# Performance work log

Hardware: AMD Instinct MI355X
Metric: run time of the kernel (lower is better)

Reference implementation:

```python
import jax, jax.numpy as jnp
import numpy as np

N, E, B = 20000, 320000, 64
H, D = 4, 64          # heads, out_channels per head
HD = H * D            # 256
F_IN = 4
NUM_ACTIONS = 100
NEG_SLOPE = 0.2


def _lin(k, fan_in, fan_out, scale=0.05):
    kw, kb = jax.random.split(k)
    return (jax.random.normal(kw, (fan_in, fan_out), jnp.float32) * scale,
            jax.random.normal(kb, (fan_out,), jnp.float32) * scale)


def setup_inputs() -> dict:
    key = jax.random.key(0)
    ks = jax.random.split(key, 32)
    x = jax.random.normal(ks[0], (N, F_IN), jnp.float32)
    edge_index = jax.random.randint(ks[1], (2, E), 0, N)
    edge_attr = jax.random.normal(ks[2], (E, 1), jnp.float32)
    batch_idx = jnp.sort(jax.random.randint(ks[3], (N,), 0, B))
    action = jax.random.randint(ks[4], (B,), 0, NUM_ACTIONS)

    # GATv2 layer 1 (in=4)
    Wl1, bl1 = _lin(ks[5], F_IN, HD)
    Wr1, br1 = _lin(ks[6], F_IN, HD)
    We1 = jax.random.normal(ks[7], (1, HD), jnp.float32) * 0.05
    att1 = jax.random.normal(ks[8], (H, D), jnp.float32) * 0.05
    b1 = jnp.zeros((HD,), jnp.float32)
    # GATv2 layer 2 (in=256)
    Wl2, bl2 = _lin(ks[9], HD, HD)
    Wr2, br2 = _lin(ks[10], HD, HD)
    We2 = jax.random.normal(ks[11], (1, HD), jnp.float32) * 0.05
    att2 = jax.random.normal(ks[12], (H, D), jnp.float32) * 0.05
    b2 = jnp.zeros((HD,), jnp.float32)
    # critic MLP 256->128->64->1
    Wc1, bc1 = _lin(ks[13], 256, 128)
    Wc2, bc2 = _lin(ks[14], 128, 64)
    Wc3, bc3 = _lin(ks[15], 64, 1)
    # actor MLP 256->128->64->num_actions
    Wa1, ba1 = _lin(ks[16], 256, 128)
    Wa2, ba2 = _lin(ks[17], 128, 64)
    Wa3, ba3 = _lin(ks[18], 64, NUM_ACTIONS)
    return dict(x=x, edge_index=edge_index, edge_attr=edge_attr, batch_idx=batch_idx,
                action=action,
                Wl1=Wl1, bl1=bl1, Wr1=Wr1, br1=br1, We1=We1, att1=att1, b1=b1,
                Wl2=Wl2, bl2=bl2, Wr2=Wr2, br2=br2, We2=We2, att2=att2, b2=b2,
                Wc1=Wc1, bc1=bc1, Wc2=Wc2, bc2=bc2, Wc3=Wc3, bc3=bc3,
                Wa1=Wa1, ba1=ba1, Wa2=Wa2, ba2=ba2, Wa3=Wa3, ba3=ba3)


def gatv2(x, src, dst, edge_attr, Wl, bl, Wr, br, We, att, bias):
    n = x.shape[0]
    xl = (x @ Wl + bl).reshape(n, H, D)   # source transform (messages)
    xr = (x @ Wr + br).reshape(n, H, D)   # target transform
    e = (edge_attr @ We).reshape(-1, H, D)
    m = xl[src] + xr[dst] + e             # [E,H,D]
    s = jnp.sum(jax.nn.leaky_relu(m, NEG_SLOPE) * att, axis=-1)  # [E,H]
    smax = jax.ops.segment_max(s, dst, num_segments=n)
    a = jnp.exp(s - smax[dst])
    denom = jax.ops.segment_sum(a, dst, num_segments=n)
    alpha = a / (denom[dst] + 1e-16)      # scatter-softmax over in-edges
    out = jax.ops.segment_sum(alpha[..., None] * xl[src], dst, num_segments=n)
    return out.reshape(n, HD) + bias


def mlp3(f, W1, b1, W2, b2, W3, b3):
    h = jax.nn.relu(f @ W1 + b1)
    h = jax.nn.relu(h @ W2 + b2)
    return h @ W3 + b3


def reference(x, edge_index, edge_attr, batch_idx, action,
              Wl1, bl1, Wr1, br1, We1, att1, b1,
              Wl2, bl2, Wr2, br2, We2, att2, b2,
              Wc1, bc1, Wc2, bc2, Wc3, bc3,
              Wa1, ba1, Wa2, ba2, Wa3, ba3):
    src, dst = edge_index[0], edge_index[1]
    h = jax.nn.relu(gatv2(x, src, dst, edge_attr, Wl1, bl1, Wr1, br1, We1, att1, b1))
    h = jax.nn.relu(gatv2(h, src, dst, edge_attr, Wl2, bl2, Wr2, br2, We2, att2, b2))
    # global mean pool over graphs
    sums = jax.ops.segment_sum(h, batch_idx, num_segments=B)
    cnts = jax.ops.segment_sum(jnp.ones((h.shape[0],), h.dtype), batch_idx, num_segments=B)
    feats = sums / jnp.maximum(cnts, 1.0)[:, None]          # [B,256]
    logits = mlp3(feats, Wa1, ba1, Wa2, ba2, Wa3, ba3)       # [B,A]
    value = mlp3(feats, Wc1, bc1, Wc2, bc2, Wc3, bc3)        # [B,1]
    logp = jax.nn.log_softmax(logits, axis=-1)
    log_prob = jnp.take_along_axis(logp, action[:, None], axis=-1)[:, 0]
    entropy = -jnp.sum(jnp.exp(logp) * logp, axis=-1)
    return logits, log_prob, entropy, value
```

## Files before the change

### kernel.cpp

```cpp
#include <hip/hip_runtime.h>
#include <hip/hip_bf16.h>
#include <cstddef>

typedef __hip_bfloat16 bf16;
typedef unsigned short u16;
typedef __attribute__((ext_vector_type(8))) short short8;
typedef __attribute__((ext_vector_type(4))) float float4v;
typedef __attribute__((ext_vector_type(2))) float float2v;

#define HD 256
#define A_MAX 128

static __device__ __forceinline__ float b2f(const bf16 v) { return __bfloat162float(v); }
static __device__ __forceinline__ bf16 f2b(float v) { return __float2bfloat16(v); }

static __device__ __forceinline__ float2v up2(unsigned int u) {
  union { unsigned int i; float f; } a, b;
  a.i = u << 16; b.i = u & 0xffff0000u;
  float2v r; r.x = a.f; r.y = b.f; return r;
}

static __device__ __forceinline__ float ldf(const void* p, size_t i, bool f32) {
  return f32 ? ((const float*)p)[i] : b2f(((const bf16*)p)[i]);
}
template <bool F32>
static __device__ __forceinline__ float ldt(const void* p, size_t i) {
  return F32 ? ((const float*)p)[i] : b2f(((const bf16*)p)[i]);
}
static __device__ __forceinline__ void stf(void* p, size_t i, bool f32, float v) {
  if (f32) ((float*)p)[i] = v;
  else     ((bf16*)p)[i] = f2b(v);
}

__global__ void k_sentinel(float* out, int n, float v) {
  int i = blockIdx.x * blockDim.x + threadIdx.x;
  if (i < n) out[i] = v;
}

__global__ void k_init(const u16* __restrict__ xbits, int* __restrict__ flag,
                       int* deg, int N) {
  int i = blockIdx.x * blockDim.x + threadIdx.x;
  if (blockIdx.x == 0 && threadIdx.x < 64) {
    int l = threadIdx.x;
    int huge = 0;
    for (int k = l; k < 256; k += 64) {
      u16 u = xbits[2 * k];
      int ex = (u >> 7) & 0xFF;
      if (ex >= 0xB0) huge++;
    }
#pragma unroll
    for (int off = 32; off > 0; off >>= 1) huge += __shfl_xor(huge, off, 64);
    if (l == 0) *flag = (huge >= 20) ? 1 : 0;
  }
  if (i < N) deg[i] = 0;
}

__global__ void k_hist(const int* __restrict__ dst, int* __restrict__ deg, int E) {
  int e = blockIdx.x * blockDim.x + threadIdx.x;
  if (e < E) atomicAdd(&deg[dst[e]], 1);
}

__global__ void k_scan(const int* __restrict__ deg, int* __restrict__ offs, int n) {
  __shared__ int wsum[17];
  __shared__ int carry_s;
  int t = threadIdx.x, w = t >> 6, l = t & 63;
  if (t == 0) carry_s = 0;
  __syncthreads();
  for (int base = 0; base < n; base += 1024) {
    int i = base + t;
    int v = (i < n) ? deg[i] : 0;
    int x = v;
#pragma unroll
    for (int off = 1; off < 64; off <<= 1) {
      int y = __shfl_up(x, off, 64);
      if (l >= off) x += y;
    }
    if (l == 63) wsum[w] = x;
    __syncthreads();
    if (t == 0) {
      int s = 0;
#pragma unroll
      for (int k = 0; k < 16; k++) { int tmp = wsum[k]; wsum[k] = s; s += tmp; }
      wsum[16] = s;
    }
    __syncthreads();
    int c = carry_s;
    if (i < n) offs[i] = c + wsum[w] + x - v;
    __syncthreads();
    if (t == 0) carry_s = c + wsum[16];
    __syncthreads();
  }
  if (t == 0) offs[n] = carry_s;
}

__global__ void k_misc(const int* __restrict__ src, const int* __restrict__ dst,
                       const void* __restrict__ ea, int* __restrict__ offs,
                       int2* __restrict__ csr,
                       const void* __restrict__ x,
                       const void* __restrict__ Wl1, const void* __restrict__ bl1,
                       const void* __restrict__ Wr1, const void* __restrict__ br1,
                       bf16* __restrict__ P, bf16* __restrict__ Q,
                       const void* __restrict__ Wl2, const void* __restrict__ Wr2,
                       const void* __restrict__ bl2, const void* __restrict__ br2,
                       bf16* __restrict__ Wfrag, bf16* __restrict__ bias2,
                       const int* __restrict__ flag,
                       int E, int N, int nSc, int nX1) {
  bool f32 = flag[0] != 0;
  int b = blockIdx.x, t = threadIdx.x;
  if (b < nSc) {
    int e = b * 256 + t;
    if (e >= E) return;
    int d = dst[e];
    int pos = atomicAdd(&offs[d], 1);
    int2 v;
    v.x = src[e];
    v.y = __float_as_int(ldf(ea, e, f32));
    csr[pos] = v;
  } else if (b < nSc + nX1) {
    int n0 = (b - nSc) * 4;
    float wl0 = ldf(Wl1, t, f32),          wl1 = ldf(Wl1, HD + t, f32);
    float wl2 = ldf(Wl1, 2 * HD + t, f32), wl3 = ldf(Wl1, 3 * HD + t, f32);
    float wr0 = ldf(Wr1, t, f32),          wr1 = ldf(Wr1, HD + t, f32);
    float wr2 = ldf(Wr1, 2 * HD + t, f32), wr3 = ldf(Wr1, 3 * HD + t, f32);
    float bbl = ldf(bl1, t, f32), bbr = ldf(br1, t, f32);
#pragma unroll
    for (int k = 0; k < 4; k++) {
      int n = n0 + k;
      if (n >= N) break;
      float x0 = ldf(x, (size_t)n * 4 + 0, f32), x1 = ldf(x, (size_t)n * 4 + 1, f32);
      float x2 = ldf(x, (size_t)n * 4 + 2, f32), x3 = ldf(x, (size_t)n * 4 + 3, f32);
      P[(size_t)n * HD + t] = f2b(bbl + x0 * wl0 + x1 * wl1 + x2 * wl2 + x3 * wl3);
      Q[(size_t)n * HD + t] = f2b(bbr + x0 * wr0 + x1 * wr1 + x2 * wr2 + x3 * wr3);
    }
  } else {
    int pb = b - nSc - nX1;
    int ct = pb >> 3, kt = pb & 7;
    if (pb == 0) {
      bias2[t]       = f2b(ldf(bl2, t, f32));
      bias2[t + 256] = f2b(ldf(br2, t, f32));
    }
#pragma unroll
    for (int half = 0; half < 2; half++) {
      int e = half * 256 + t;
      int m = e & 15;
      int rest = e >> 4;
      int quad = rest >> 3, j = rest & 7;
      int l = quad * 16 + m;
      int k = kt * 32 + quad * 8 + j;
      int n = ct * 16 + m;
      const void* W = (n < 256) ? Wl2 : Wr2;
      float v = ldf(W, (size_t)k * 256 + (n & 255), f32);
      Wfrag[(size_t)pb * 512 + l * 8 + j] = f2b(v);
    }
  }
}

__global__ __launch_bounds__(256) void k_xform2_mfma(
    const bf16* __restrict__ hin, const bf16* __restrict__ Wfrag,
    const bf16* __restrict__ bias2,
    bf16* __restrict__ P, bf16* __restrict__ Q, int N) {
  int w = threadIdx.x >> 6, l = threadIdx.x & 63;
  int r0 = blockIdx.x * 16;
  if (r0 >= N) return;
  int m = l & 15;
  int quad = l >> 4;
  int row = r0 + m;
  if (row >= N) row = N - 1;

  short8 a[8];
  const u16* arow = (const u16*)hin + (size_t)row * 256;
#pragma unroll
  for (int kt = 0; kt < 8; kt++)
    a[kt] = *(const short8*)(arow + kt * 32 + quad * 8);

#pragma unroll
  for (int ct = 0; ct < 8; ct++) {
    int c_tile = w * 8 + ct;
    int c = c_tile * 16 + m;
    const u16* bbase = (const u16*)Wfrag + ((size_t)c_tile * 8) * 512 + l * 8;
    float4v acc = {0.f, 0.f, 0.f, 0.f};
#pragma unroll
    for (int kt = 0; kt < 8; kt++) {
      short8 b = *(const short8*)(bbase + kt * 512);
      acc = __builtin_amdgcn_mfma_f32_16x16x32_bf16(a[kt], b, acc, 0, 0, 0);
    }
    float bv = b2f(bias2[c]);
#pragma unroll
    for (int i = 0; i < 4; i++) {
      int r = r0 + quad * 4 + i;
      if (r < N) {
        float v = acc[i] + bv;
        if (c < 256) P[(size_t)r * 256 + c] = f2b(v);
        else         Q[(size_t)r * 256 + (c - 256)] = f2b(v);
      }
    }
  }
}

__global__ __launch_bounds__(256) void k_gat(
    const bf16* __restrict__ xl, const bf16* __restrict__ xr,
    const int2* __restrict__ csr, const int* __restrict__ offs,
    const void* __restrict__ We, const void* __restrict__ att,
    const void* __restrict__ bias,
    bf16* __restrict__ hout, const int* __restrict__ flag, int N) {
  int w = threadIdx.x >> 6, l = threadIdx.x & 63;
  int n = blockIdx.x * 4 + w;
  if (n >= N) return;
  bool f32 = flag[0] != 0;
  int d0 = l << 2;

  uint2 xu = *(const uint2*)((const u16*)xr + (size_t)n * HD + d0);
  float2v xr01 = up2(xu.x), xr23 = up2(xu.y);
  float2v We01, We23, at01, at23;
  We01.x = ldf(We, d0 + 0, f32); We01.y = ldf(We, d0 + 1, f32);
  We23.x = ldf(We, d0 + 2, f32); We23.y = ldf(We, d0 + 3, f32);
  at01.x = ldf(att, d0 + 0, f32); at01.y = ldf(att, d0 + 1, f32);
  at23.x = ldf(att, d0 + 2, f32); at23.y = ldf(att, d0 + 3, f32);

  int beg = (n > 0) ? offs[n - 1] : 0;
  int end = offs[n];
  float2v acc01 = {0.f, 0.f}, acc23 = {0.f, 0.f};
  float dn = 0.f;

  int j = beg;
  for (; j + 4 <= end; j += 4) {
    int2 v[4];
#pragma unroll
    for (int q = 0; q < 4; q++) v[q] = csr[j + q];
    uint2 su[4];
#pragma unroll
    for (int q = 0; q < 4; q++)
      su[q] = *(const uint2*)((const u16*)xl + (size_t)v[q].x * HD + d0);
    float2v x01[4], x23[4];
    float ps[4];
#pragma unroll
    for (int q = 0; q < 4; q++) {
      x01[q] = up2(su[q].x); x23[q] = up2(su[q].y);
      float eav = __int_as_float(v[q].y);
      float2v ev; ev.x = eav; ev.y = eav;
      float2v m01 = x01[q] + xr01 + ev * We01;
      float2v m23 = x23[q] + xr23 + ev * We23;
      float2v lr01, lr23;
      lr01.x = fmaxf(m01.x, 0.2f * m01.x); lr01.y = fmaxf(m01.y, 0.2f * m01.y);
      lr23.x = fmaxf(m23.x, 0.2f * m23.x); lr23.y = fmaxf(m23.y, 0.2f * m23.y);
      float2v pp = lr01 * at01 + lr23 * at23;
      ps[q] = pp.x + pp.y;
    }
#pragma unroll
    for (int off = 1; off <= 8; off <<= 1) {
#pragma unroll
      for (int q = 0; q < 4; q++) ps[q] += __shfl_xor(ps[q], off, 64);
    }
#pragma unroll
    for (int q = 0; q < 4; q++) {
      float a = __expf(fminf(fmaxf(ps[q], -40.f), 40.f));
      dn += a;
      float2v av; av.x = a; av.y = a;
      acc01 += av * x01[q];
      acc23 += av * x23[q];
    }
  }
  for (; j < end; j++) {
    int2 v = csr[j];
    float eav = __int_as_float(v.y);
    uint2 su = *(const uint2*)((const u16*)xl + (size_t)v.x * HD + d0);
    float2v x01 = up2(su.x), x23 = up2(su.y);
    float2v ev; ev.x = eav; ev.y = eav;
    float2v m01 = x01 + xr01 + ev * We01;
    float2v m23 = x23 + xr23 + ev * We23;
    float2v lr01, lr23;
    lr01.x = fmaxf(m01.x, 0.2f * m01.x); lr01.y = fmaxf(m01.y, 0.2f * m01.y);
    lr23.x = fmaxf(m23.x, 0.2f * m23.x); lr23.y = fmaxf(m23.y, 0.2f * m23.y);
    float2v pp = lr01 * at01 + lr23 * at23;
    float ps = pp.x + pp.y;
    ps += __shfl_xor(ps, 1, 64);
    ps += __shfl_xor(ps, 2, 64);
    ps += __shfl_xor(ps, 4, 64);
    ps += __shfl_xor(ps, 8, 64);
    float a = __expf(fminf(fmaxf(ps, -40.f), 40.f));
    dn += a;
    float2v av; av.x = a; av.y = a;
    acc01 += av * x01;
    acc23 += av * x23;
  }

  float inv = 1.f / (dn + 1e-16f);
  bf16 o[4];
  o[0] = f2b(fmaxf(acc01.x * inv + ldf(bias, d0 + 0, f32), 0.f));
  o[1] = f2b(fmaxf(acc01.y * inv + ldf(bias, d0 + 1, f32), 0.f));
  o[2] = f2b(fmaxf(acc23.x * inv + ldf(bias, d0 + 2, f32), 0.f));
  o[3] = f2b(fmaxf(acc23.y * inv + ldf(bias, d0 + 3, f32), 0.f));
  *(ushort4*)((u16*)hout + (size_t)n * HD + d0) = *(ushort4*)o;
}


static __device__ __forceinline__ int lb(const int* a, int n, int v) {
  int lo = 0, hi = n;
  while (lo < hi) { int m = (lo + hi) >> 1; if (a[m] < v) lo = m + 1; else hi = m; }
  return lo;
}

template <bool F32>
static __device__ void mlp_body(const bf16* __restrict__ R,
                                const int* __restrict__ bidx, int N,
                                const int* __restrict__ act,
                                const void* Wa1, const void* ba1, const void* Wa2, const void* ba2,
                                const void* Wa3, const void* ba3,
                                const void* Wc1, const void* bc1, const void* Wc2, const void* bc2,
                                const void* Wc3, const void* bc3,
                                void* __restrict__ out, int B, int A) {
  __shared__ float f[HD];
  __shared__ float p1[2][128];
  __shared__ float h1[128];
  __shared__ float p2[4][64];
  __shared__ float h2[64];
  __shared__ float lg[A_MAX];
  __shared__ float sc[2];
  int blk = blockIdx.x, g = blk >> 1, which = blk & 1, t = threadIdx.x;
  int s_ = lb(bidx, N, g), e_ = lb(bidx, N, g + 1);
  float inv = 1.f / fmaxf((float)(e_ - s_), 1.f);
  {
    float a0 = 0.f, a1 = 0.f, a2 = 0.f, a3 = 0.f;
    int i = s_;
    for (; i + 4 <= e_; i += 4) {
      a0 += b2f(R[(size_t)(i + 0) * HD + t]);
      a1 += b2f(R[(size_t)(i + 1) * HD + t]);
      a2 += b2f(R[(size_t)(i + 2) * HD + t]);
      a3 += b2f(R[(size_t)(i + 3) * HD + t]);
    }
    for (; i < e_; i++) a0 += b2f(R[(size_t)i * HD + t]);
    f[t] = ((a0 + a1) + (a2 + a3)) * inv;
  }
  __syncthreads();

  const void *W1 = which ? Wc1 : Wa1, *B1 = which ? bc1 : ba1;
  const void *W2 = which ? Wc2 : Wa2, *B2 = which ? bc2 : ba2;

  {
    int j = t & 127, half = t >> 7;
    int i0 = half * 128;
    float a0 = 0.f, a1 = 0.f, a2 = 0.f, a3 = 0.f;
    for (int u = 0; u < 128; u += 4) {
      a0 += f[i0 + u + 0] * ldt<F32>(W1, (size_t)(i0 + u + 0) * 128 + j);
      a1 += f[i0 + u + 1] * ldt<F32>(W1, (size_t)(i0 + u + 1) * 128 + j);
      a2 += f[i0 + u + 2] * ldt<F32>(W1, (size_t)(i0 + u + 2) * 128 + j);
      a3 += f[i0 + u + 3] * ldt<F32>(W1, (size_t)(i0 + u + 3) * 128 + j);
    }
    p1[half][j] = (a0 + a1) + (a2 + a3);
  }
  __syncthreads();
  if (t < 128) h1[t] = fmaxf(p1[0][t] + p1[1][t] + ldt<F32>(B1, t), 0.f);
  __syncthreads();

  {
    int j = t & 63, q = t >> 6;
    int i0 = q * 32;
    float a0 = 0.f, a1 = 0.f;
    for (int u = 0; u < 32; u += 2) {
      a0 += h1[i0 + u + 0] * ldt<F32>(W2, (size_t)(i0 + u + 0) * 64 + j);
      a1 += h1[i0 + u + 1] * ldt<F32>(W2, (size_t)(i0 + u + 1) * 64 + j);
    }
    p2[q][j] = a0 + a1;
  }
  __syncthreads();
  if (t < 64) h2[t] = fmaxf(p2[0][t] + p2[1][t] + p2[2][t] + p2[3][t] + ldt<F32>(B2, t), 0.f);
  __syncthreads();

  if (which == 0) {
    if (t < A) {
      float a0 = 0.f, a1 = 0.f, a2 = 0.f, a3 = 0.f;
      for (int i = 0; i < 64; i += 4) {
        a0 += h2[i + 0] * ldt<F32>(Wa3, (size_t)(i + 0) * A + t);
        a1 += h2[i + 1] * ldt<F32>(Wa3, (size_t)(i + 1) * A + t);
        a2 += h2[i + 2] * ldt<F32>(Wa3, (size_t)(i + 2) * A + t);
        a3 += h2[i + 3] * ldt<F32>(Wa3, (size_t)(i + 3) * A + t);
      }
      lg[t] = (a0 + a1) + (a2 + a3) + ldt<F32>(ba3, t);
    }
    __syncthreads();
    if (t == 0) {
      float mx = -3.4e38f;
      for (int i = 0; i < A; i++) mx = fmaxf(mx, lg[i]);
      float s = 0.f;
      for (int i = 0; i < A; i++) s += __expf(lg[i] - mx);
      sc[0] = mx;
      sc[1] = logf(s);
    }
    __syncthreads();
    float mx = sc[0], lse = sc[1];
    if (t < A) stf(out, (size_t)g * A + t, F32, lg[t]);
    if (t == 0) {
      int a = act[g];
      stf(out, (size_t)B * A + g, F32, lg[a] - mx - lse);
      float ent = 0.f;
      for (int i = 0; i < A; i++) {
        float l = lg[i] - mx - lse;
        ent -= __expf(l) * l;
      }
      stf(out, (size_t)B * A + B + g, F32, ent);
    }
  } else {
    if (t < 64) {
      float v = h2[t] * ldt<F32>(Wc3, t);
#pragma unroll
      for (int off = 32; off > 0; off >>= 1) v += __shfl_xor(v, off, 64);
      if (t == 0) stf(out, (size_t)B * A + 2 * B + g, F32, v + ldt<F32>(bc3, 0));
    }
  }
}

__global__ void k_mlp(const bf16* __restrict__ R,
                      const int* __restrict__ bidx, int N,
                      const int* __restrict__ act,
                      const void* Wa1, const void* ba1, const void* Wa2, const void* ba2,
                      const void* Wa3, const void* ba3,
                      const void* Wc1, const void* bc1, const void* Wc2, const void* bc2,
                      const void* Wc3, const void* bc3,
                      void* __restrict__ out, const int* __restrict__ flag, int B, int A) {
  if (flag[0] != 0)
    mlp_body<true >(R, bidx, N, act, Wa1, ba1, Wa2, ba2, Wa3, ba3,
                    Wc1, bc1, Wc2, bc2, Wc3, bc3, out, B, A);
  else
    mlp_body<false>(R, bidx, N, act, Wa1, ba1, Wa2, ba2, Wa3, ba3,
                    Wc1, bc1, Wc2, bc2, Wc3, bc3, out, B, A);
}


extern "C" void kernel_launch(void* const* d_in, const int* in_sizes, int n_in,
                              void* d_out, int out_size, void* d_ws, size_t ws_size,
                              hipStream_t stream) {
  const void* x    = d_in[0];
  const int*  ei   = (const int*)d_in[1];
  const void* ea   = d_in[2];
  const int*  bidx = (const int*)d_in[3];
  const int*  act  = (const int*)d_in[4];
  const void *Wl1 = d_in[5],  *bl1 = d_in[6];
  const void *Wr1 = d_in[7],  *br1 = d_in[8];
  const void *We1 = d_in[9],  *att1 = d_in[10];
  const void *b1  = d_in[11];
  const void *Wl2 = d_in[12], *bl2 = d_in[13];
  const void *Wr2 = d_in[14], *br2 = d_in[15];
  const void *We2 = d_in[16], *att2 = d_in[17];
  const void *b2  = d_in[18];
  const void *Wc1 = d_in[19], *bc1 = d_in[20];
  const void *Wc2 = d_in[21], *bc2 = d_in[22];
  const void *Wc3 = d_in[23], *bc3 = d_in[24];
  const void *Wa1 = d_in[25], *ba1 = d_in[26];
  const void *Wa2 = d_in[27], *ba2 = d_in[28];
  const void *Wa3 = d_in[29], *ba3 = d_in[30];

  const int N = in_sizes[0] / 4;
  const int E = in_sizes[1] / 2;
  const int B = in_sizes[4];
  const int A = in_sizes[30];

  char* p = (char*)d_ws;
  auto carve = [&](size_t bytes) {
    void* r = (void*)p;
    p += (bytes + 255) & ~(size_t)255;
    return r;
  };
  int*   dflag   = (int*)carve(4);
  int*   deg     = (int*)carve((size_t)N * 4);
  int*   offs    = (int*)carve((size_t)(N + 1) * 4);
  int2*  csr     = (int2*)carve((size_t)E * 8);
  bf16*  P       = (bf16*)carve((size_t)N * HD * 2);
  bf16*  Q       = (bf16*)carve((size_t)N * HD * 2);
  bf16*  R       = (bf16*)carve((size_t)N * HD * 2);
  bf16*  Wfrag   = (bf16*)carve((size_t)512 * 256 * 2);
  bf16*  bias2   = (bf16*)carve((size_t)512 * 2);
  size_t need = (size_t)(p - (char*)d_ws);

  if (ws_size < need) {
    float v = 1000.f + (float)(ws_size >> 20);
    int n = out_size / 2;
    k_sentinel<<<(n + 255) / 256, 256, 0, stream>>>((float*)d_out, n, v);
    return;
  }

  const int* srcA = ei;
  const int* dstA = ei + E;

  int nSc = (E + 255) / 256;
  int nX1 = (N + 3) / 4;

  k_init<<<(N + 255) / 256, 256, 0, stream>>>((const u16*)x, dflag, deg, N);
  k_hist<<<(E + 255) / 256, 256, 0, stream>>>(dstA, deg, E);
  k_scan<<<1, 1024, 0, stream>>>(deg, offs, N);
  k_misc<<<nSc + nX1 + 256, 256, 0, stream>>>(srcA, dstA, ea, offs, csr,
                                              x, Wl1, bl1, Wr1, br1, P, Q,
                                              Wl2, Wr2, bl2, br2, Wfrag, bias2,
                                              dflag, E, N, nSc, nX1);
  k_gat<<<(N + 3) / 4, 256, 0, stream>>>(P, Q, csr, offs, We1, att1, b1, R, dflag, N);
  k_xform2_mfma<<<(N + 15) / 16, 256, 0, stream>>>(R, Wfrag, bias2, P, Q, N);
  k_gat<<<(N + 3) / 4, 256, 0, stream>>>(P, Q, csr, offs, We2, att2, b2, R, dflag, N);
  k_mlp<<<B * 2, 256, 0, stream>>>(R, bidx, N, act,
                                   Wa1, ba1, Wa2, ba2, Wa3, ba3,
                                   Wc1, bc1, Wc2, bc2, Wc3, bc3,
                                   d_out, dflag, B, A);
}
```

Before: 318.8 us.

## Parallelize degree scan across blocks and split mean-pool into separate kernel

Replaces the single-block serial prefix scan over node degrees with a three-kernel block-sum, block-offset and apply scan spread over many blocks. Moves global mean pooling out of the MLP kernel into a new pooling kernel where 16 blocks per graph each sum a strided subset of nodes into fp32 partials, which the MLP kernel then reduces. Both changes target serial phases that ran on few blocks. In exchange they add three extra kernel launches and a small partial-sum buffer in the workspace.

```diff
diff --git a/kernel.cpp b/kernel.cpp
--- a/kernel.cpp
+++ b/kernel.cpp
@@ -60,37 +60,53 @@
   if (e < E) atomicAdd(&deg[dst[e]], 1);
 }
 
-__global__ void k_scan(const int* __restrict__ deg, int* __restrict__ offs, int n) {
-  __shared__ int wsum[17];
-  __shared__ int carry_s;
-  int t = threadIdx.x, w = t >> 6, l = t & 63;
-  if (t == 0) carry_s = 0;
-  __syncthreads();
-  for (int base = 0; base < n; base += 1024) {
-    int i = base + t;
-    int v = (i < n) ? deg[i] : 0;
-    int x = v;
-#pragma unroll
-    for (int off = 1; off < 64; off <<= 1) {
-      int y = __shfl_up(x, off, 64);
-      if (l >= off) x += y;
-    }
-    if (l == 63) wsum[w] = x;
-    __syncthreads();
-    if (t == 0) {
-      int s = 0;
-#pragma unroll
-      for (int k = 0; k < 16; k++) { int tmp = wsum[k]; wsum[k] = s; s += tmp; }
-      wsum[16] = s;
-    }
-    __syncthreads();
-    int c = carry_s;
-    if (i < n) offs[i] = c + wsum[w] + x - v;
-    __syncthreads();
-    if (t == 0) carry_s = c + wsum[16];
-    __syncthreads();
-  }
-  if (t == 0) offs[n] = carry_s;
+__global__ void k_sumb(const int* __restrict__ deg, int* __restrict__ bsum, int n) {
+  __shared__ int ws[16];
+  int b = blockIdx.x, t = threadIdx.x;
+  int i = b * 1024 + t;
+  int v = (i < n) ? deg[i] : 0;
+#pragma unroll
+  for (int off = 32; off > 0; off >>= 1) v += __shfl_xor(v, off, 64);
+  if ((t & 63) == 0) ws[t >> 6] = v;
+  __syncthreads();
+  if (t == 0) {
+    int s = 0;
+#pragma unroll
+    for (int k = 0; k < 16; k++) s += ws[k];
+    bsum[b] = s;
+  }
+}
+
+__global__ void k_scanb(const int* __restrict__ bsum, int* __restrict__ boff,
+                        int nb, int* __restrict__ offs, int n) {
+  if (threadIdx.x == 0) {
+    int s = 0;
+    for (int i = 0; i < nb; i++) { boff[i] = s; s += bsum[i]; }
+    offs[n] = s;
+  }
+}
+
+__global__ void k_scanapply(const int* __restrict__ deg, const int* __restrict__ boff,
+                            int* __restrict__ offs, int n) {
+  __shared__ int wsum[16];
+  int b = blockIdx.x, t = threadIdx.x, w = t >> 6, l = t & 63;
+  int i = b * 1024 + t;
+  int v = (i < n) ? deg[i] : 0;
+  int x = v;
+#pragma unroll
+  for (int off = 1; off < 64; off <<= 1) {
+    int y = __shfl_up(x, off, 64);
+    if (l >= off) x += y;
+  }
+  if (l == 63) wsum[w] = x;
+  __syncthreads();
+  if (t == 0) {
+    int s = 0;
+#pragma unroll
+    for (int k = 0; k < 16; k++) { int tmp = wsum[k]; wsum[k] = s; s += tmp; }
+  }
+  __syncthreads();
+  if (i < n) offs[i] = boff[b] + wsum[w] + x - v;
 }
 
 __global__ void k_misc(const int* __restrict__ src, const int* __restrict__ dst,
@@ -300,8 +316,25 @@
   return lo;
 }
 
+__global__ void k_pool(const bf16* __restrict__ h, const int* __restrict__ bidx,
+                       float* __restrict__ feats16, int Bc, int N) {
+  int g = blockIdx.x >> 4, part = blockIdx.x & 15, t = threadIdx.x;
+  int s = lb(bidx, N, g), e_ = lb(bidx, N, g + 1);
+  float a0 = 0.f, a1 = 0.f, a2 = 0.f, a3 = 0.f;
+  int i = s + part;
+  for (; i + 48 < e_; i += 64) {
+    a0 += b2f(h[(size_t)(i +  0) * HD + t]);
+    a1 += b2f(h[(size_t)(i + 16) * HD + t]);
+    a2 += b2f(h[(size_t)(i + 32) * HD + t]);
+    a3 += b2f(h[(size_t)(i + 48) * HD + t]);
+  }
+  for (; i < e_; i += 16) a0 += b2f(h[(size_t)i * HD + t]);
+  feats16[((size_t)part * Bc + g) * HD + t] = (a0 + a1) + (a2 + a3);
+}
+
+
 template <bool F32>
-static __device__ void mlp_body(const bf16* __restrict__ R,
+static __device__ void mlp_body(const float* __restrict__ feats16,
                                 const int* __restrict__ bidx, int N,
                                 const int* __restrict__ act,
                                 const void* Wa1, const void* ba1, const void* Wa2, const void* ba2,
@@ -320,16 +353,15 @@
   int s_ = lb(bidx, N, g), e_ = lb(bidx, N, g + 1);
   float inv = 1.f / fmaxf((float)(e_ - s_), 1.f);
   {
-    float a0 = 0.f, a1 = 0.f, a2 = 0.f, a3 = 0.f;
-    int i = s_;
-    for (; i + 4 <= e_; i += 4) {
-      a0 += b2f(R[(size_t)(i + 0) * HD + t]);
-      a1 += b2f(R[(size_t)(i + 1) * HD + t]);
-      a2 += b2f(R[(size_t)(i + 2) * HD + t]);
-      a3 += b2f(R[(size_t)(i + 3) * HD + t]);
-    }
-    for (; i < e_; i++) a0 += b2f(R[(size_t)i * HD + t]);
-    f[t] = ((a0 + a1) + (a2 + a3)) * inv;
+    float s0 = 0.f, s1 = 0.f, s2 = 0.f, s3 = 0.f;
+#pragma unroll
+    for (int pp = 0; pp < 16; pp += 4) {
+      s0 += feats16[((size_t)(pp + 0) * B + g) * HD + t];
+      s1 += feats16[((size_t)(pp + 1) * B + g) * HD + t];
+      s2 += feats16[((size_t)(pp + 2) * B + g) * HD + t];
+      s3 += feats16[((size_t)(pp + 3) * B + g) * HD + t];
+    }
+    f[t] = ((s0 + s1) + (s2 + s3)) * inv;
   }
   __syncthreads();
 
@@ -409,7 +441,7 @@
   }
 }
 
-__global__ void k_mlp(const bf16* __restrict__ R,
+__global__ void k_mlp(const float* __restrict__ feats16,
                       const int* __restrict__ bidx, int N,
                       const int* __restrict__ act,
                       const void* Wa1, const void* ba1, const void* Wa2, const void* ba2,
@@ -418,10 +450,10 @@
                       const void* Wc3, const void* bc3,
                       void* __restrict__ out, const int* __restrict__ flag, int B, int A) {
   if (flag[0] != 0)
-    mlp_body<true >(R, bidx, N, act, Wa1, ba1, Wa2, ba2, Wa3, ba3,
+    mlp_body<true >(feats16, bidx, N, act, Wa1, ba1, Wa2, ba2, Wa3, ba3,
                     Wc1, bc1, Wc2, bc2, Wc3, bc3, out, B, A);
   else
-    mlp_body<false>(R, bidx, N, act, Wa1, ba1, Wa2, ba2, Wa3, ba3,
+    mlp_body<false>(feats16, bidx, N, act, Wa1, ba1, Wa2, ba2, Wa3, ba3,
                     Wc1, bc1, Wc2, bc2, Wc3, bc3, out, B, A);
 }
 
@@ -469,6 +501,10 @@
   bf16*  R       = (bf16*)carve((size_t)N * HD * 2);
   bf16*  Wfrag   = (bf16*)carve((size_t)512 * 256 * 2);
   bf16*  bias2   = (bf16*)carve((size_t)512 * 2);
+  float* feats16 = (float*)carve((size_t)16 * B * HD * 4);
+  int    nb      = (N + 1023) / 1024;
+  int*   bsum    = (int*)carve((size_t)nb * 4);
+  int*   boff    = (int*)carve((size_t)nb * 4);
   size_t need = (size_t)(p - (char*)d_ws);
 
   if (ws_size < need) {
@@ -486,7 +522,9 @@
 
   k_init<<<(N + 255) / 256, 256, 0, stream>>>((const u16*)x, dflag, deg, N);
   k_hist<<<(E + 255) / 256, 256, 0, stream>>>(dstA, deg, E);
-  k_scan<<<1, 1024, 0, stream>>>(deg, offs, N);
+  k_sumb<<<nb, 1024, 0, stream>>>(deg, bsum, N);
+  k_scanb<<<1, 64, 0, stream>>>(bsum, boff, nb, offs, N);
+  k_scanapply<<<nb, 1024, 0, stream>>>(deg, boff, offs, N);
   k_misc<<<nSc + nX1 + 256, 256, 0, stream>>>(srcA, dstA, ea, offs, csr,
                                               x, Wl1, bl1, Wr1, br1, P, Q,
                                               Wl2, Wr2, bl2, br2, Wfrag, bias2,
@@ -494,7 +532,8 @@
   k_gat<<<(N + 3) / 4, 256, 0, stream>>>(P, Q, csr, offs, We1, att1, b1, R, dflag, N);
   k_xform2_mfma<<<(N + 15) / 16, 256, 0, stream>>>(R, Wfrag, bias2, P, Q, N);
   k_gat<<<(N + 3) / 4, 256, 0, stream>>>(P, Q, csr, offs, We2, att2, b2, R, dflag, N);
-  k_mlp<<<B * 2, 256, 0, stream>>>(R, bidx, N, act,
+  k_pool<<<B * 16, 256, 0, stream>>>(R, bidx, feats16, B, N);
+  k_mlp<<<B * 2, 256, 0, stream>>>(feats16, bidx, N, act,
                                    Wa1, ba1, Wa2, ba2, Wa3, ba3,
                                    Wc1, bc1, Wc2, bc2, Wc3, bc3,
                                    d_out, dflag, B, A);
```

New measurement: 290.2 us (median of 2 runs). 9.0% less time.
